# Optimization experiments

Hardware: AMD Instinct MI355X
Metric: run time of the kernel (lower is better)

## Reference

```python
import jax, jax.numpy as jnp
import numpy as np
from jax import lax

K = 2       # kernel_size
STRIDE = 2  # stride (== kernel_size by default)


def setup_inputs() -> dict:
    key = jax.random.key(0)
    k1, k2, k3 = jax.random.split(key, 3)
    x = jax.random.normal(k1, (16, 192, 224, 224), dtype=jnp.float32)
    w_avg = jax.random.uniform(k2, (1, 192, 1, 1), dtype=jnp.float32)
    w_max = jax.random.uniform(k3, (1, 192, 1, 1), dtype=jnp.float32)
    return {"x": x, "w_avg": w_avg, "w_max": w_max}


def reference(x, w_avg, w_max):
    # CombPool2d, coefficient_type='channelwise':
    #   out = (w_avg**2) * avg_pool(x) + (w_max**2) * max_pool(x)
    # Window over spatial dims of NCHW input; no padding, dilation=1.
    win = (1, 1, K, K)
    strides = (1, 1, STRIDE, STRIDE)
    avg = lax.reduce_window(x, 0.0, lax.add, win, strides, 'VALID') / (K * K)
    mx = lax.reduce_window(x, -jnp.inf, lax.max, win, strides, 'VALID')
    # coefficients (1,C,1,1) broadcast over (B,C,H',W')
    return (w_avg ** 2) * avg + (w_max ** 2) * mx
```

## Files before the change

### kernel.cpp

```cpp
#include <hip/hip_runtime.h>


typedef float f4 __attribute__((ext_vector_type(4)));

#define IN_HW   (224 * 224)
#define OUT_HW  (112 * 112)
#define NCH     192

__global__ __launch_bounds__(256) void combpool2d_kernel(
    const float* __restrict__ x,
    const float* __restrict__ w_avg,
    const float* __restrict__ w_max,
    float* __restrict__ out,
    int n4)
{
    int stride = gridDim.x * blockDim.x;
    for (int i = blockIdx.x * blockDim.x + threadIdx.x; i < n4; i += stride) {
        int ow4 = i % 28;
        int t   = i / 28;
        int oh  = t % 112;
        int bc  = t / 112;
        int c   = bc % NCH;

        const float* row0 = x + (size_t)bc * IN_HW + (size_t)(2 * oh) * 224;
        const f4* r0 = (const f4*)row0;
        const f4* r1 = (const f4*)(row0 + 224);

        f4 a0 = __builtin_nontemporal_load(&r0[2 * ow4]);
        f4 a1 = __builtin_nontemporal_load(&r0[2 * ow4 + 1]);
        f4 b0 = __builtin_nontemporal_load(&r1[2 * ow4]);
        f4 b1 = __builtin_nontemporal_load(&r1[2 * ow4 + 1]);

        float ca = w_avg[c]; ca *= ca;
        float cm = w_max[c]; cm *= cm;

        f4 o;
        o.x = ca * (0.25f * ((a0.x + a0.y) + (b0.x + b0.y)))
            + cm * fmaxf(fmaxf(a0.x, a0.y), fmaxf(b0.x, b0.y));
        o.y = ca * (0.25f * ((a0.z + a0.w) + (b0.z + b0.w)))
            + cm * fmaxf(fmaxf(a0.z, a0.w), fmaxf(b0.z, b0.w));
        o.z = ca * (0.25f * ((a1.x + a1.y) + (b1.x + b1.y)))
            + cm * fmaxf(fmaxf(a1.x, a1.y), fmaxf(b1.x, b1.y));
        o.w = ca * (0.25f * ((a1.z + a1.w) + (b1.z + b1.w)))
            + cm * fmaxf(fmaxf(a1.z, a1.w), fmaxf(b1.z, b1.w));

        f4* orow = (f4*)(out + (size_t)bc * OUT_HW + (size_t)oh * 112);
        __builtin_nontemporal_store(o, &orow[ow4]);
    }
}

extern "C" void kernel_launch(void* const* d_in, const int* in_sizes, int n_in,
                              void* d_out, int out_size, void* d_ws, size_t ws_size,
                              hipStream_t stream) {
    const float* x     = (const float*)d_in[0];
    const float* w_avg = (const float*)d_in[1];
    const float* w_max = (const float*)d_in[2];
    float* out = (float*)d_out;

    int n4 = out_size / 4;
    int block = 256;
    int grid = (n4 + block - 1) / block;
    if (grid > 2048) grid = 2048;
    combpool2d_kernel<<<grid, block, 0, stream>>>(x, w_avg, w_max, out, n4);
}
```

Before: 798.3 us.

## Remap thread-to-data access for contiguous loads and launch one thread per item

Each thread now reads f4 at q and q+28 in each input row rather than two adjacent f4s, so neighbouring lanes load contiguous 16-byte chunks. It writes two f2 outputs at q and q+28. Loads become ordinary cached loads instead of nontemporal ones. The grid-stride loop and the 2048-block cap are removed so every output item gets its own thread. The aim is better coalescing and more memory parallelism, at the cost of narrower 8-byte stores and a much larger grid.

After: 815.0 us. +2.1%, slower.

```diff
diff --git a/kernel.cpp b/kernel.cpp
--- a/kernel.cpp
+++ b/kernel.cpp
@@ -2,6 +2,7 @@
 
 
 typedef float f4 __attribute__((ext_vector_type(4)));
+typedef float f2 __attribute__((ext_vector_type(2)));
 
 #define IN_HW   (224 * 224)
 #define OUT_HW  (112 * 112)
@@ -14,39 +15,40 @@
     float* __restrict__ out,
     int n4)
 {
-    int stride = gridDim.x * blockDim.x;
-    for (int i = blockIdx.x * blockDim.x + threadIdx.x; i < n4; i += stride) {
-        int ow4 = i % 28;
-        int t   = i / 28;
-        int oh  = t % 112;
-        int bc  = t / 112;
-        int c   = bc % NCH;
+    int i = blockIdx.x * blockDim.x + threadIdx.x;
+    if (i >= n4) return;
 
-        const float* row0 = x + (size_t)bc * IN_HW + (size_t)(2 * oh) * 224;
-        const f4* r0 = (const f4*)row0;
-        const f4* r1 = (const f4*)(row0 + 224);
+    int q  = i % 28;
+    int t  = i / 28;
+    int oh = t % 112;
+    int bc = t / 112;
+    int c  = bc % NCH;
 
-        f4 a0 = __builtin_nontemporal_load(&r0[2 * ow4]);
-        f4 a1 = __builtin_nontemporal_load(&r0[2 * ow4 + 1]);
-        f4 b0 = __builtin_nontemporal_load(&r1[2 * ow4]);
-        f4 b1 = __builtin_nontemporal_load(&r1[2 * ow4 + 1]);
+    const float* row0 = x + (size_t)bc * IN_HW + (size_t)(2 * oh) * 224;
+    const f4* r0 = (const f4*)row0;
+    const f4* r1 = (const f4*)(row0 + 224);
 
-        float ca = w_avg[c]; ca *= ca;
-        float cm = w_max[c]; cm *= cm;
+    f4 a0 = r0[q];
+    f4 a1 = r0[q + 28];
+    f4 b0 = r1[q];
+    f4 b1 = r1[q + 28];
 
-        f4 o;
-        o.x = ca * (0.25f * ((a0.x + a0.y) + (b0.x + b0.y)))
-            + cm * fmaxf(fmaxf(a0.x, a0.y), fmaxf(b0.x, b0.y));
-        o.y = ca * (0.25f * ((a0.z + a0.w) + (b0.z + b0.w)))
-            + cm * fmaxf(fmaxf(a0.z, a0.w), fmaxf(b0.z, b0.w));
-        o.z = ca * (0.25f * ((a1.x + a1.y) + (b1.x + b1.y)))
-            + cm * fmaxf(fmaxf(a1.x, a1.y), fmaxf(b1.x, b1.y));
-        o.w = ca * (0.25f * ((a1.z + a1.w) + (b1.z + b1.w)))
-            + cm * fmaxf(fmaxf(a1.z, a1.w), fmaxf(b1.z, b1.w));
+    float ca = w_avg[c]; ca *= ca;
+    float cm = w_max[c]; cm *= cm;
 
-        f4* orow = (f4*)(out + (size_t)bc * OUT_HW + (size_t)oh * 112);
-        __builtin_nontemporal_store(o, &orow[ow4]);
-    }
+    f2 o0, o1;
+    o0.x = ca * (0.25f * ((a0.x + a0.y) + (b0.x + b0.y)))
+         + cm * fmaxf(fmaxf(a0.x, a0.y), fmaxf(b0.x, b0.y));
+    o0.y = ca * (0.25f * ((a0.z + a0.w) + (b0.z + b0.w)))
+         + cm * fmaxf(fmaxf(a0.z, a0.w), fmaxf(b0.z, b0.w));
+    o1.x = ca * (0.25f * ((a1.x + a1.y) + (b1.x + b1.y)))
+         + cm * fmaxf(fmaxf(a1.x, a1.y), fmaxf(b1.x, b1.y));
+    o1.y = ca * (0.25f * ((a1.z + a1.w) + (b1.z + b1.w)))
+         + cm * fmaxf(fmaxf(a1.z, a1.w), fmaxf(b1.z, b1.w));
+
+    f2* orow = (f2*)(out + (size_t)bc * OUT_HW + (size_t)oh * 112);
+    __builtin_nontemporal_store(o0, &orow[q]);
+    __builtin_nontemporal_store(o1, &orow[q + 28]);
 }
 
 extern "C" void kernel_launch(void* const* d_in, const int* in_sizes, int n_in,
@@ -60,6 +62,5 @@
     int n4 = out_size / 4;
     int block = 256;
     int grid = (n4 + block - 1) / block;
-    if (grid > 2048) grid = 2048;
     combpool2d_kernel<<<grid, block, 0, stream>>>(x, w_avg, w_max, out, n4);
 }
```
